# Kernel tuning notes

Hardware: AMD Instinct MI355X
Metric: run time of the kernel (lower is better)

## Reference

```python
import jax, jax.numpy as jnp
import numpy as np

B, S, HID, NH = 4, 2048, 1024, 16
HD = HID // NH  # head_dim = 64


def setup_inputs() -> dict:
    key = jax.random.key(0)
    ks = jax.random.split(key, 5)
    scale = 0.02
    return {
        "hidden_states": jax.random.normal(ks[0], (B, S, HID), dtype=jnp.float32),
        "attention_mask": jnp.zeros((B, 1, 1, S), dtype=jnp.float32),
        "Wq": jax.random.normal(ks[1], (HID, HID), dtype=jnp.float32) * scale,
        "bq": jnp.zeros((HID,), dtype=jnp.float32),
        "Wk": jax.random.normal(ks[2], (HID, HID), dtype=jnp.float32) * scale,
        "bk": jnp.zeros((HID,), dtype=jnp.float32),
        "Wv": jax.random.normal(ks[3], (HID, HID), dtype=jnp.float32) * scale,
        "bv": jnp.zeros((HID,), dtype=jnp.float32),
    }


def _split_heads(x):
    # [B, S, HID] -> [B, NH, S, HD]
    b, s, _ = x.shape
    return x.reshape(b, s, NH, HD).transpose(0, 2, 1, 3)


def reference(hidden_states, attention_mask, Wq, bq, Wk, bk, Wv, bv):
    # Linear projections (torch Linear: x @ W.T + b)
    q = _split_heads(hidden_states @ Wq.T + bq)
    k = _split_heads(hidden_states @ Wk.T + bk)
    v = _split_heads(hidden_states @ Wv.T + bv)

    # scores: [B, NH, S, S]
    scores = jnp.einsum("bhqd,bhkd->bhqk", q, k) / jnp.sqrt(jnp.float32(HD))
    scores = scores + attention_mask  # additive mask, broadcast over heads/query
    weights = jax.nn.softmax(scores, axis=-1)
    # dropout prob = 0 (inference), head_mask = None

    context = jnp.einsum("bhqk,bhkd->bhqd", weights, v)
    # [B, NH, S, HD] -> [B, S, HID]
    context = context.transpose(0, 2, 1, 3).reshape(hidden_states.shape[0], hidden_states.shape[1], HID)
    return context
```

## Files before the change

kernel.cpp:

```cpp
#include <hip/hip_runtime.h>
#include <stdint.h>


typedef float f32x4 __attribute__((ext_vector_type(4)));
typedef float f32x16 __attribute__((ext_vector_type(16)));
typedef __bf16 bf16x8 __attribute__((ext_vector_type(8)));
typedef unsigned short ushort_t;
typedef uint32_t u32;

#define MFMA16(a, b, c) __builtin_amdgcn_mfma_f32_16x16x32_bf16(a, b, c, 0, 0, 0)
#define MFMA32(a, b, c) __builtin_amdgcn_mfma_f32_32x32x16_bf16(a, b, c, 0, 0, 0)

__device__ __forceinline__ ushort_t f2b(float f) {
    union { float f; uint32_t u; } x{f};
    uint32_t r = (x.u + 0x7fffu + ((x.u >> 16) & 1u)) >> 16;
    return (ushort_t)r;
}

__device__ __forceinline__ float fexp2(float x) {
#if __has_builtin(__builtin_amdgcn_exp2f)
    return __builtin_amdgcn_exp2f(x);
#else
    return exp2f(x);
#endif
}

__device__ __forceinline__ u32 pkpair(float e, float o) {
    union { float f; u32 u; } xe{e}, xo{o};
    return __builtin_amdgcn_perm(xo.u, xe.u, 0x07060302u);
}

__device__ __forceinline__ bf16x8 mk8(u32 a, u32 b, u32 c, u32 d) {
    union { u32 u[4]; bf16x8 v; } x;
    x.u[0] = a; x.u[1] = b; x.u[2] = c; x.u[3] = d;
    return x.v;
}

__device__ __forceinline__ void gld_lds16(const void* g, void* l) {
    __builtin_amdgcn_global_load_lds(
        (const __attribute__((address_space(1))) unsigned int*)g,
        (__attribute__((address_space(3))) unsigned int*)l, 16, 0, 0);
}

__global__ __launch_bounds__(256) void convert_k(
    const float* __restrict__ hs, const float* __restrict__ wq,
    const float* __restrict__ wk, const float* __restrict__ wv,
    ushort_t* __restrict__ hs_b, ushort_t* __restrict__ w_b) {
    size_t c = (size_t)blockIdx.x * 256 + threadIdx.x;
    size_t i = c * 8;
    const size_t NHS = (size_t)8192 * 1024;
    const float* src;
    ushort_t* dst;
    if (i < NHS) { src = hs + i; dst = hs_b + i; }
    else {
        size_t j = i - NHS;
        int w = (int)(j >> 20);
        size_t o = j & ((1u << 20) - 1);
        src = (w == 0 ? wq : (w == 1 ? wk : wv)) + o;
        dst = w_b + ((size_t)w << 20) + o;
    }
    float4 a = *(const float4*)src;
    float4 b = *(const float4*)(src + 4);
    uint32_t p0 = (uint32_t)f2b(a.x) | ((uint32_t)f2b(a.y) << 16);
    uint32_t p1 = (uint32_t)f2b(a.z) | ((uint32_t)f2b(a.w) << 16);
    uint32_t p2 = (uint32_t)f2b(b.x) | ((uint32_t)f2b(b.y) << 16);
    uint32_t p3 = (uint32_t)f2b(b.z) | ((uint32_t)f2b(b.w) << 16);
    uint4 v{p0, p1, p2, p3};
    *(uint4*)dst = v;
}

__global__ __launch_bounds__(256, 2) void qkv_gemm(
    const ushort_t* __restrict__ Ab, const ushort_t* __restrict__ Wb,
    const float* __restrict__ bq, const float* __restrict__ bk,
    const float* __restrict__ bv, ushort_t* __restrict__ q_ws,
    ushort_t* __restrict__ k_ws, ushort_t* __restrict__ vt_ws) {
    __shared__ __align__(16) char smem_raw[128 * 136 * 2];
    ushort_t* At = (ushort_t*)smem_raw;
    ushort_t* Bt = At + 128 * 64;
    ushort_t* Ct = (ushort_t*)smem_raw;
    int which = blockIdx.z;
    const ushort_t* W = Wb + ((size_t)which << 20);
    int m0 = blockIdx.y * 128, n0 = blockIdx.x * 128;
    int t = threadIdx.x, lane = t & 63, wave = t >> 6;
    int quad = lane >> 4, l16 = lane & 15;
    int wr = (wave >> 1) * 64, wc = (wave & 1) * 64;
    f32x4 acc[4][4] = {};
    for (int k0 = 0; k0 < 1024; k0 += 64) {
        for (int r = 0; r < 4; r++) {
            int idx = r * 256 + t;
            int row = idx >> 3, co = (idx & 7) * 8;
            gld_lds16(Ab + (size_t)(m0 + row) * 1024 + k0 + co, At + idx * 8);
            gld_lds16(W + (size_t)(n0 + row) * 1024 + k0 + co, Bt + idx * 8);
        }
        asm volatile("s_waitcnt vmcnt(0)" ::: "memory");
        __syncthreads();
        for (int kk = 0; kk < 2; kk++) {
            bf16x8 af[4], bf[4];
            for (int i = 0; i < 4; i++)
                af[i] = *(const bf16x8*)(At + (wr + i * 16 + l16) * 64 + kk * 32 + quad * 8);
            for (int j = 0; j < 4; j++)
                bf[j] = *(const bf16x8*)(Bt + (wc + j * 16 + l16) * 64 + kk * 32 + quad * 8);
            for (int i = 0; i < 4; i++)
                for (int j = 0; j < 4; j++)
                    acc[i][j] = MFMA16(af[i], bf[j], acc[i][j]);
        }
        __syncthreads();
    }
    const float* bias = which == 0 ? bq : (which == 1 ? bk : bv);
    float sc = which == 0 ? (0.125f * 1.44269504f) : 1.0f;
    if (which == 2) {
        for (int j = 0; j < 4; j++) {
            float bias_v = bias[n0 + wc + j * 16 + l16];
            for (int i = 0; i < 4; i++) {
                ushort4 pk;
                pk.x = f2b(acc[i][j].x + bias_v);
                pk.y = f2b(acc[i][j].y + bias_v);
                pk.z = f2b(acc[i][j].z + bias_v);
                pk.w = f2b(acc[i][j].w + bias_v);
                *(ushort4*)(Ct + (wc + j * 16 + l16) * 136 + wr + i * 16 + quad * 4) = pk;
            }
        }
    } else {
        for (int j = 0; j < 4; j++) {
            float bias_v = bias[n0 + wc + j * 16 + l16];
            int col = wc + j * 16 + l16;
            for (int i = 0; i < 4; i++) {
                int rb = wr + i * 16 + quad * 4;
                Ct[(rb + 0) * 136 + col] = f2b((acc[i][j].x + bias_v) * sc);
                Ct[(rb + 1) * 136 + col] = f2b((acc[i][j].y + bias_v) * sc);
                Ct[(rb + 2) * 136 + col] = f2b((acc[i][j].z + bias_v) * sc);
                Ct[(rb + 3) * 136 + col] = f2b((acc[i][j].w + bias_v) * sc);
            }
        }
    }
    __syncthreads();
    for (int r = 0; r < 8; r++) {
        int idx = r * 256 + t;
        int row = idx >> 4, c8 = (idx & 15) * 8;
        uint4 val = *(const uint4*)(Ct + row * 136 + c8);
        if (which == 2) {
            int col = n0 + row, h = col >> 6, d = col & 63;
            int tok = m0 + c8, b = tok >> 11, s = tok & 2047;
            *(uint4*)(vt_ws + ((size_t)(b * 16 + h) * 64 + d) * 2048 + s) = val;
        } else {
            int tok = m0 + row, b = tok >> 11, s = tok & 2047;
            int col = n0 + c8, h = col >> 6, d = col & 63;
            ushort_t* base = which == 0 ? q_ws : k_ws;
            *(uint4*)(base + ((size_t)(b * 16 + h) * 2048 + s) * 64 + d) = val;
        }
    }
}

__global__ __launch_bounds__(256, 2) void attn_k(
    const ushort_t* __restrict__ q_ws, const ushort_t* __restrict__ k_ws,
    const ushort_t* __restrict__ vt_ws, const float* __restrict__ mask,
    float* __restrict__ out) {
    __shared__ __align__(16) char smraw[33280];
    ushort_t* Kl = (ushort_t*)smraw;
    ushort_t* Vtl = Kl + 64 * 64;
    float* Ow = (float*)smraw;

    int bh = blockIdx.y, b = bh >> 4, h = bh & 15;
    int q0 = blockIdx.x * 256;
    int t = threadIdx.x, lane = t & 63, w = t >> 6;
    int l31 = lane & 31, hi = lane >> 5;
    bool h0 = (hi == 0);
    const ushort_t* Q = q_ws + (size_t)bh * 2048 * 64;
    const ushort_t* K = k_ws + (size_t)bh * 2048 * 64;
    const ushort_t* Vt = vt_ws + (size_t)bh * 64 * 2048;
    const float* mrow = mask + b * 2048;

    bf16x8 qf[2][4];
#pragma unroll
    for (int qg = 0; qg < 2; qg++)
#pragma unroll
        for (int cs = 0; cs < 4; cs++)
            qf[qg][cs] = *(const bf16x8*)(
                Q + (size_t)(q0 + w * 64 + qg * 32 + l31) * 64 + cs * 16 + hi * 8);
    int co[4];
#pragma unroll
    for (int cs = 0; cs < 4; cs++) co[cs] = ((cs * 2 + hi) ^ (l31 & 7)) * 8;

    f32x16 o00 = {}, o01 = {}, o10 = {}, o11 = {};
    float rs0 = 0.f, rs1 = 0.f;

    for (int t0 = 0; t0 < 2048; t0 += 64) {
#pragma unroll
        for (int it = 0; it < 2; it++) {
            int idx = it * 256 + t;
            int row = idx >> 3, ch = idx & 7;
            int sch = (ch ^ (row & 7)) * 8;
            gld_lds16(K + (size_t)(t0 + row) * 64 + sch, Kl + idx * 8);
            gld_lds16(Vt + (size_t)row * 2048 + t0 + sch, Vtl + idx * 8);
        }
        asm volatile("s_waitcnt vmcnt(0)" ::: "memory");
        __syncthreads();
        f32x16 s00 = {}, s01 = {}, s10 = {}, s11 = {};
#pragma unroll
        for (int cs = 0; cs < 4; cs++) {
            bf16x8 k0 = *(const bf16x8*)(Kl + l31 * 64 + co[cs]);
            bf16x8 k1 = *(const bf16x8*)(Kl + (32 + l31) * 64 + co[cs]);
            s00 = MFMA32(k0, qf[0][cs], s00);
            s01 = MFMA32(k1, qf[0][cs], s01);
            s10 = MFMA32(k0, qf[1][cs], s10);
            s11 = MFMA32(k1, qf[1][cs], s11);
        }
        bf16x8 pfr[2][4];
#pragma unroll
        for (int qg = 0; qg < 2; qg++) {
            const f32x16& sa = qg ? s10 : s00;
            const f32x16& sb = qg ? s11 : s01;
            u32 pa[8], pb[8];
            float rst = 0.f;
#pragma unroll
            for (int i = 0; i < 4; i++) {
                float4 bm = *(const float4*)(mrow + t0 + 8 * i + 4 * hi);
                float e0 = fexp2(fmaf(bm.x, 1.44269504f, sa[4 * i + 0]));
                float e1 = fexp2(fmaf(bm.y, 1.44269504f, sa[4 * i + 1]));
                float e2 = fexp2(fmaf(bm.z, 1.44269504f, sa[4 * i + 2]));
                float e3 = fexp2(fmaf(bm.w, 1.44269504f, sa[4 * i + 3]));
                rst += (e0 + e1) + (e2 + e3);
                pa[2 * i] = pkpair(e0, e1);
                pa[2 * i + 1] = pkpair(e2, e3);
            }
#pragma unroll
            for (int i = 0; i < 4; i++) {
                float4 bm = *(const float4*)(mrow + t0 + 32 + 8 * i + 4 * hi);
                float e0 = fexp2(fmaf(bm.x, 1.44269504f, sb[4 * i + 0]));
                float e1 = fexp2(fmaf(bm.y, 1.44269504f, sb[4 * i + 1]));
                float e2 = fexp2(fmaf(bm.z, 1.44269504f, sb[4 * i + 2]));
                float e3 = fexp2(fmaf(bm.w, 1.44269504f, sb[4 * i + 3]));
                rst += (e0 + e1) + (e2 + e3);
                pb[2 * i] = pkpair(e0, e1);
                pb[2 * i + 1] = pkpair(e2, e3);
            }
            if (qg == 0) rs0 += rst; else rs1 += rst;
#pragma unroll
            for (int g = 0; g < 4; g++) {
                const u32* aa = (g < 2) ? pa : pb;
                int base = (g & 1) * 4;
                u32 y0 = h0 ? aa[base + 2] : aa[base + 0];
                u32 y1 = h0 ? aa[base + 3] : aa[base + 1];
                u32 sy0 = (u32)__shfl_xor((int)y0, 32, 64);
                u32 sy1 = (u32)__shfl_xor((int)y1, 32, 64);
                pfr[qg][g] = mk8(h0 ? aa[base + 0] : sy0, h0 ? aa[base + 1] : sy1,
                                 h0 ? sy0 : aa[base + 2], h0 ? sy1 : aa[base + 3]);
            }
        }
#pragma unroll
        for (int cs = 0; cs < 4; cs++) {
            bf16x8 v0 = *(const bf16x8*)(Vtl + l31 * 64 + co[cs]);
            bf16x8 v1 = *(const bf16x8*)(Vtl + (32 + l31) * 64 + co[cs]);
            o00 = MFMA32(v0, pfr[0][cs], o00);
            o01 = MFMA32(v1, pfr[0][cs], o01);
            o10 = MFMA32(v0, pfr[1][cs], o10);
            o11 = MFMA32(v1, pfr[1][cs], o11);
        }
        __syncthreads();
    }
    rs0 += __shfl_xor(rs0, 32, 64);
    rs1 += __shfl_xor(rs1, 32, 64);
    float inv0 = 1.f / rs0, inv1 = 1.f / rs1;
#pragma unroll
    for (int qg = 0; qg < 2; qg++) {
        float inv = qg ? inv1 : inv0;
        const f32x16& a0 = qg ? o10 : o00;
        const f32x16& a1 = qg ? o11 : o01;
#pragma unroll
        for (int g = 0; g < 4; g++) {
            f32x4 c0, c1;
#pragma unroll
            for (int r = 0; r < 4; r++) {
                c0[r] = a0[4 * g + r] * inv;
                c1[r] = a1[4 * g + r] * inv;
            }
            *(f32x4*)(Ow + (w * 32 + l31) * 65 + 8 * g + 4 * hi) = c0;
            *(f32x4*)(Ow + (w * 32 + l31) * 65 + 32 + 8 * g + 4 * hi) = c1;
        }
        __syncthreads();
#pragma unroll
        for (int cc = 0; cc < 8; cc++) {
            int c = cc * 256 + t;
            int row = c >> 4, seg = (c & 15) * 4;
            f32x4 vv = *(const f32x4*)(Ow + row * 65 + seg);
            int ql = (row >> 5) * 64 + qg * 32 + (row & 31);
            *(f32x4*)(out + ((size_t)(b * 2048 + q0 + ql)) * 1024 + h * 64 + seg) = vv;
        }
        __syncthreads();
    }
}

extern "C" void kernel_launch(void* const* d_in, const int* in_sizes, int n_in,
                              void* d_out, int out_size, void* d_ws, size_t ws_size,
                              hipStream_t stream) {
    const float* hs = (const float*)d_in[0];
    const float* mask = (const float*)d_in[1];
    const float* wq = (const float*)d_in[2];
    const float* bq = (const float*)d_in[3];
    const float* wk = (const float*)d_in[4];
    const float* bk = (const float*)d_in[5];
    const float* wv = (const float*)d_in[6];
    const float* bv = (const float*)d_in[7];
    float* out = (float*)d_out;
    char* ws = (char*)d_ws;
    ushort_t* hs_b = (ushort_t*)ws;
    ushort_t* w_b = (ushort_t*)(ws + 16777216);
    ushort_t* q_ws = (ushort_t*)(ws + 23068672);
    ushort_t* k_ws = (ushort_t*)(ws + 39845888);
    ushort_t* vt_ws = (ushort_t*)(ws + 56623104);

    convert_k<<<5632, 256, 0, stream>>>(hs, wq, wk, wv, hs_b, w_b);
    qkv_gemm<<<dim3(8, 64, 3), 256, 0, stream>>>(hs_b, w_b, bq, bk, bv, q_ws, k_ws, vt_ws);
    attn_k<<<dim3(8, 64), 256, 0, stream>>>(q_ws, k_ws, vt_ws, mask, out);
}
```

Measured before the change: 259.3 us.

## Double-buffer K/V tiles in attention and drop P-fragment shuffles

```diff
diff --git a/kernel.cpp b/kernel.cpp
--- a/kernel.cpp
+++ b/kernel.cpp
@@ -4,6 +4,7 @@
 
 typedef float f32x4 __attribute__((ext_vector_type(4)));
 typedef float f32x16 __attribute__((ext_vector_type(16)));
+typedef __bf16 bf16x4 __attribute__((ext_vector_type(4)));
 typedef __bf16 bf16x8 __attribute__((ext_vector_type(8)));
 typedef unsigned short ushort_t;
 typedef uint32_t u32;
@@ -34,6 +35,10 @@
     union { u32 u[4]; bf16x8 v; } x;
     x.u[0] = a; x.u[1] = b; x.u[2] = c; x.u[3] = d;
     return x.v;
+}
+
+__device__ __forceinline__ bf16x8 cat8(bf16x4 a, bf16x4 b) {
+    return __builtin_shufflevector(a, b, 0, 1, 2, 3, 4, 5, 6, 7);
 }
 
 __device__ __forceinline__ void gld_lds16(const void* g, void* l) {
@@ -156,15 +161,12 @@
     const ushort_t* __restrict__ vt_ws, const float* __restrict__ mask,
     float* __restrict__ out) {
     __shared__ __align__(16) char smraw[33280];
-    ushort_t* Kl = (ushort_t*)smraw;
-    ushort_t* Vtl = Kl + 64 * 64;
     float* Ow = (float*)smraw;
 
     int bh = blockIdx.y, b = bh >> 4, h = bh & 15;
     int q0 = blockIdx.x * 256;
     int t = threadIdx.x, lane = t & 63, w = t >> 6;
     int l31 = lane & 31, hi = lane >> 5;
-    bool h0 = (hi == 0);
     const ushort_t* Q = q_ws + (size_t)bh * 2048 * 64;
     const ushort_t* K = k_ws + (size_t)bh * 2048 * 64;
     const ushort_t* Vt = vt_ws + (size_t)bh * 64 * 2048;
@@ -184,18 +186,30 @@
     f32x16 o00 = {}, o01 = {}, o10 = {}, o11 = {};
     float rs0 = 0.f, rs1 = 0.f;
 
-    for (int t0 = 0; t0 < 2048; t0 += 64) {
+    auto stage = [&](int buf, int t0) {
+        ushort_t* Kb = (ushort_t*)smraw + buf * 8192;
 #pragma unroll
         for (int it = 0; it < 2; it++) {
             int idx = it * 256 + t;
             int row = idx >> 3, ch = idx & 7;
             int sch = (ch ^ (row & 7)) * 8;
-            gld_lds16(K + (size_t)(t0 + row) * 64 + sch, Kl + idx * 8);
-            gld_lds16(Vt + (size_t)row * 2048 + t0 + sch, Vtl + idx * 8);
-        }
-        asm volatile("s_waitcnt vmcnt(0)" ::: "memory");
-        __syncthreads();
+            gld_lds16(K + (size_t)(t0 + row) * 64 + sch, Kb + idx * 8);
+            gld_lds16(Vt + (size_t)row * 2048 + t0 + sch, Kb + 4096 + idx * 8);
+        }
+    };
+
+    stage(0, 0);
+    asm volatile("s_waitcnt vmcnt(0)" ::: "memory");
+    __syncthreads();
+    int cur = 0;
+
+    for (int t0 = 0; t0 < 2048; t0 += 64) {
+        if (t0 + 64 < 2048) stage(cur ^ 1, t0 + 64);
+        const ushort_t* Kl = (const ushort_t*)smraw + cur * 8192;
+        const ushort_t* Vtl = Kl + 4096;
+
         f32x16 s00 = {}, s01 = {}, s10 = {}, s11 = {};
+        __builtin_amdgcn_s_setprio(1);
 #pragma unroll
         for (int cs = 0; cs < 4; cs++) {
             bf16x8 k0 = *(const bf16x8*)(Kl + l31 * 64 + co[cs]);
@@ -205,6 +219,8 @@
             s10 = MFMA32(k0, qf[1][cs], s10);
             s11 = MFMA32(k1, qf[1][cs], s11);
         }
+        __builtin_amdgcn_s_setprio(0);
+
         bf16x8 pfr[2][4];
 #pragma unroll
         for (int qg = 0; qg < 2; qg++) {
@@ -235,28 +251,31 @@
                 pb[2 * i + 1] = pkpair(e2, e3);
             }
             if (qg == 0) rs0 += rst; else rs1 += rst;
-#pragma unroll
-            for (int g = 0; g < 4; g++) {
-                const u32* aa = (g < 2) ? pa : pb;
-                int base = (g & 1) * 4;
-                u32 y0 = h0 ? aa[base + 2] : aa[base + 0];
-                u32 y1 = h0 ? aa[base + 3] : aa[base + 1];
-                u32 sy0 = (u32)__shfl_xor((int)y0, 32, 64);
-                u32 sy1 = (u32)__shfl_xor((int)y1, 32, 64);
-                pfr[qg][g] = mk8(h0 ? aa[base + 0] : sy0, h0 ? aa[base + 1] : sy1,
-                                 h0 ? sy0 : aa[base + 2], h0 ? sy1 : aa[base + 3]);
-            }
-        }
+            pfr[qg][0] = mk8(pa[0], pa[1], pa[2], pa[3]);
+            pfr[qg][1] = mk8(pa[4], pa[5], pa[6], pa[7]);
+            pfr[qg][2] = mk8(pb[0], pb[1], pb[2], pb[3]);
+            pfr[qg][3] = mk8(pb[4], pb[5], pb[6], pb[7]);
+        }
+
+        __builtin_amdgcn_s_setprio(1);
 #pragma unroll
         for (int cs = 0; cs < 4; cs++) {
-            bf16x8 v0 = *(const bf16x8*)(Vtl + l31 * 64 + co[cs]);
-            bf16x8 v1 = *(const bf16x8*)(Vtl + (32 + l31) * 64 + co[cs]);
+            int b0 = ((2 * cs) ^ (l31 & 7)) * 8 + 4 * hi;
+            int b1 = ((2 * cs + 1) ^ (l31 & 7)) * 8 + 4 * hi;
+            bf16x8 v0 = cat8(*(const bf16x4*)(Vtl + l31 * 64 + b0),
+                             *(const bf16x4*)(Vtl + l31 * 64 + b1));
+            bf16x8 v1 = cat8(*(const bf16x4*)(Vtl + (32 + l31) * 64 + b0),
+                             *(const bf16x4*)(Vtl + (32 + l31) * 64 + b1));
             o00 = MFMA32(v0, pfr[0][cs], o00);
             o01 = MFMA32(v1, pfr[0][cs], o01);
             o10 = MFMA32(v0, pfr[1][cs], o10);
             o11 = MFMA32(v1, pfr[1][cs], o11);
         }
-        __syncthreads();
+        __builtin_amdgcn_s_setprio(0);
+
+        asm volatile("s_waitcnt vmcnt(0)" ::: "memory");
+        __syncthreads();
+        cur ^= 1;
     }
     rs0 += __shfl_xor(rs0, 32, 64);
     rs1 += __shfl_xor(rs1, 32, 64);
```

Measured after the change: 289.0 us. 1.11x slower.
